# Performance work log

Measured on AMD Instinct MI355X. Metric: run time of the kernel, lower is better.

The kernel has to match this reference:

```python
import jax, jax.numpy as jnp
import numpy as np

TEMPERATURE = 0.07
NORM_EPS = 1e-12  # matches torch F.normalize eps


def setup_inputs() -> dict:
    key = jax.random.key(0)
    k1, k2 = jax.random.split(key)
    emb = jax.random.normal(k1, (4, 256, 61, 61), dtype=jnp.float32)
    targets = jax.random.randint(k2, (4, 61, 61), 0, 5, dtype=jnp.int64)
    return {"emb": emb, "targets": targets}


def reference(emb, targets):
    n, c, h, w = emb.shape
    # (N,C,H,W) -> (N*H*W, C), L2-normalized per pixel
    feats = emb.transpose(0, 2, 3, 1).reshape(-1, c)
    norms = jnp.maximum(jnp.linalg.norm(feats, axis=1, keepdims=True), NORM_EPS)
    feats = feats / norms
    labels = targets.reshape(-1)  # (T,)
    T = labels.shape[0]

    sim = jnp.matmul(feats, feats.T) / TEMPERATURE  # (T,T)
    exp_sim = jnp.exp(sim)

    eye = jnp.eye(T, dtype=bool)
    pos_mask = (labels[None, :] == labels[:, None]) & ~eye  # (T,T) bool

    sum_pos = jnp.sum(jnp.where(pos_mask, exp_sim, 0.0), axis=1)  # (T,)
    sum_all = exp_sim.sum(axis=1) - jnp.exp(jnp.diagonal(sim))    # (T,)

    valid = sum_pos > 0
    # safe log: substitute 1.0 where invalid to avoid -inf/NaN, then mask
    safe_pos = jnp.where(valid, sum_pos, 1.0)
    safe_all = jnp.where(valid, sum_all, 1.0)
    per_row = jnp.where(valid, -(jnp.log(safe_pos) - jnp.log(safe_all)), 0.0)
    loss = per_row.sum() / jnp.maximum(valid.sum(), 1).astype(per_row.dtype)
    return loss
```

## Files before the change

### kernel.cpp

```cpp
#include <hip/hip_runtime.h>
#include <cstdint>
#include <cstddef>

#define T_REAL 14884
#define TPAD   15360
#define CDIM   256
#define HW     3721
#define NRB    60
#define NSL    16
#define TPS    15
#define NT     240
#define NPADJ  476.0f

static constexpr float SQRT_SCALE = 4.53981598f;

typedef _Float16 f16x8  __attribute__((ext_vector_type(8)));
typedef float    f32x16 __attribute__((ext_vector_type(16)));

__device__ __forceinline__ float exp2_fast(float x) {
#if __has_builtin(__builtin_amdgcn_exp2f)
    return __builtin_amdgcn_exp2f(x);
#else
    return exp2f(x);
#endif
}

#define OFF_FEATS 0u
#define SZ_FEATS  ((unsigned)TPAD * CDIM * 2u)
#define OFF_LAB   (OFF_FEATS + SZ_FEATS)
#define OFF_RANK  (OFF_LAB + (unsigned)TPAD * 4u)
#define OFF_CTL   (OFF_RANK + 59648u)
#define OFF_TCL   (OFF_CTL + 128u)
#define OFF_PART  (OFF_TCL + 1024u)
#define SZ_PART   ((unsigned)NRB * NSL * 256u * 8u)
#define OFF_ACC   (OFF_PART + SZ_PART)


__global__ void k_zero(int* __restrict__ ctl, float* __restrict__ accum) {
    int t = threadIdx.x;
    if (t < 32) ctl[t] = 0;
    if (t == 32) { accum[0] = 0.f; accum[1] = 0.f; }
}

__global__ void k_hist(const int* __restrict__ targets, int* __restrict__ ctl) {
    __shared__ int lh[5];
    const int tid = threadIdx.x;
    const int t = blockIdx.x * 256 + tid;
    if (tid < 5) lh[tid] = 0;
    __syncthreads();
    if (t < T_REAL) atomicAdd(&lh[targets[t]], 1);
    __syncthreads();
    if (tid < 5) atomicAdd(&ctl[tid], lh[tid]);
}

__global__ void k_scan(int* __restrict__ ctl, int* __restrict__ tcl,
                       int* __restrict__ labels) {
    __shared__ int soffs[6];
    const int tid = threadIdx.x;
    if (tid == 0) {
        int o = 0;
        for (int c = 0; c < 5; ++c) {
            soffs[c] = o; ctl[16 + c] = o; ctl[8 + c] = o;
            o += ctl[c];
        }
        soffs[5] = o; ctl[21] = o;
    }
    __syncthreads();
    for (int t = tid; t < NT; t += 256) {
        const int lo = t * 64, hi = lo + 64;
        int tc = -2;
        if (lo >= T_REAL) tc = -1;
        else {
#pragma unroll
            for (int c = 0; c < 5; ++c)
                if (lo >= soffs[c] && hi <= soffs[c + 1]) tc = c;
        }
        tcl[t] = tc;
    }
    for (int t = T_REAL + tid; t < TPAD; t += 256) labels[t] = -1;
}

__global__ void k_rank(const int* __restrict__ targets, int* __restrict__ ctl,
                       int* __restrict__ rank, int* __restrict__ labels) {
    const int tid = threadIdx.x;
    const int t = blockIdx.x * 256 + tid;
    const int lane = tid & 63;
    const int c = (t < T_REAL) ? targets[t] : -1;
#pragma unroll
    for (int cl = 0; cl < 5; ++cl) {
        unsigned long long m = __ballot(c == cl);
        if (c == cl) {
            const int leader = __ffsll((unsigned long long)m) - 1;
            int base = 0;
            if (lane == leader) base = atomicAdd(&ctl[8 + cl], (int)__popcll(m));
            base = __shfl(base, leader);
            const unsigned long long below = m & ((1ull << lane) - 1ull);
            const int r = base + (int)__popcll(below);
            rank[t] = r;
            labels[r] = c;
        }
    }
}

__global__ void k_prep(const float* __restrict__ emb, const int* __restrict__ rank,
                       _Float16* __restrict__ feats) {
    const int tid = threadIdx.x;
    const int bx = blockIdx.x, n = blockIdx.y;

    if (bx == 59) {
        const int r0 = T_REAL + n * 119;
        f16x8 z = {0, 0, 0, 0, 0, 0, 0, 0};
        for (int c = tid; c < 119 * 32; c += 256) {
            int rr = r0 + (c >> 5), cc = c & 31;
            *reinterpret_cast<f16x8*>(feats + (size_t)rr * CDIM + cc * 8) = z;
        }
        return;
    }

    __shared__ float tile[64][257];
    __shared__ float sspart[4][64];
    const int lane = tid & 63, w = tid >> 6;
    const int px0 = bx * 64;
    const int hw = px0 + lane;

    float ssq = 0.f;
    for (int ci = w; ci < CDIM; ci += 4) {
        float v = (hw < HW) ? emb[((size_t)(n * CDIM + ci)) * HW + hw] : 0.f;
        tile[lane][ci] = v;
        ssq += v * v;
    }
    sspart[w][lane] = ssq;
    __syncthreads();

    const int pp = tid >> 2, q = tid & 3;
    float s2 = sspart[q][pp];
    s2 += __shfl_xor(s2, 1);
    s2 += __shfl_xor(s2, 2);
    const float inv = SQRT_SCALE / fmaxf(sqrtf(s2), 1e-12f);

    const int hwp = px0 + pp;
    if (hwp < HW) {
        const int row = rank[n * HW + hwp];
        _Float16* dst = feats + (size_t)row * CDIM + q * 64;
#pragma unroll
        for (int g = 0; g < 8; ++g) {
            const int gg = g ^ q;
            f16x8 o;
#pragma unroll
            for (int e = 0; e < 8; ++e) o[e] = (_Float16)(tile[pp][q * 64 + gg * 8 + e] * inv);
            *reinterpret_cast<f16x8*>(dst + gg * 8) = o;
        }
    }
}

__device__ __forceinline__ void stage_tile(const _Float16* __restrict__ feats, int jbase,
                                           _Float16* bufp, int tid) {
#pragma unroll
    for (int sweep = 0; sweep < 8; ++sweep) {
        int ch = sweep * 256 + tid;
        int j  = ch >> 5;
        int c  = ch & 31;
        int swz = (j & 7) ^ (((j >> 3) & 3) << 1);
        int csrc = c ^ swz;
        const _Float16* src = feats + ((size_t)(jbase + j)) * CDIM + csrc * 8;
        __builtin_amdgcn_global_load_lds(
            (const __attribute__((address_space(1))) void*)src,
            (__attribute__((address_space(3))) void*)(bufp + (size_t)ch * 8),
            16, 0, 0);
    }
}

__global__ __launch_bounds__(256, 2) void k_main(const _Float16* __restrict__ feats,
                                                 const int* __restrict__ labels,
                                                 const int* __restrict__ tcl,
                                                 float2* __restrict__ partials) {
    __shared__ __align__(16) _Float16 buf[2][64 * 256];
    const int tid  = threadIdx.x;
    const int w    = tid >> 6, lane = tid & 63;
    const int lo   = lane & 31, hi = lane >> 5;
    const int rb = blockIdx.x, slice = blockIdx.y;
    const int ibase = rb * 256 + w * 64;

    const int labi0 = labels[ibase + lo];
    const int labi1 = labels[ibase + 32 + lo];

    f16x8 b0[16], b1[16];
    {
        const f16x8* r0 = (const f16x8*)(feats + (size_t)(ibase + lo) * CDIM + hi * 8);
        const f16x8* r1 = (const f16x8*)(feats + (size_t)(ibase + 32 + lo) * CDIM + hi * 8);
#pragma unroll
        for (int ks = 0; ks < 16; ++ks) { b0[ks] = r0[ks * 2]; b1[ks] = r1[ks * 2]; }
    }

    const int s  = (lo & 7) ^ (((lo >> 3) & 3) << 1);
    const int sp = s >> 1;
    const int x0h = (s & 1) << 3;
    int idx4[4];
#pragma unroll
    for (int m = 0; m < 4; ++m)
        idx4[m] = lo * 256 + ((hi << 3) ^ x0h) + (((m ^ sp)) << 4);

    float accA0 = 0.f, accP0 = 0.f, accA1 = 0.f, accP1 = 0.f;

    stage_tile(feats, slice * 64, &buf[0][0], tid);

#pragma unroll 1
    for (int ti = 0; ti < TPS; ++ti) {
        const int jt = slice + ti * NSL;

        __builtin_amdgcn_s_barrier();
        __builtin_amdgcn_sched_barrier(0);
        if (ti + 1 < TPS) {
            stage_tile(feats, (jt + NSL) * 64, &buf[(ti + 1) & 1][0], tid);
            asm volatile("s_waitcnt vmcnt(8)" ::: "memory");
        } else {
            asm volatile("s_waitcnt vmcnt(0)" ::: "memory");
        }
        __builtin_amdgcn_s_barrier();
        __builtin_amdgcn_sched_barrier(0);

        const _Float16* bc = &buf[ti & 1][0];
        const int tc = tcl[jt];
        float tT0 = 0.f, tT1 = 0.f;

#pragma unroll
        for (int jg = 0; jg < 2; ++jg) {
            const _Float16* bjg = bc + jg * 8192;
            f32x16 cA = {0,0,0,0,0,0,0,0,0,0,0,0,0,0,0,0};
            f32x16 cB = cA;
#pragma unroll
            for (int ks = 0; ks < 16; ++ks) {
                const f16x8 a = *reinterpret_cast<const f16x8*>(
                    bjg + idx4[ks & 3] + ((ks & 12) << 4));
                cA = __builtin_amdgcn_mfma_f32_32x32x16_f16(a, b0[ks], cA, 0, 0, 0);
                cB = __builtin_amdgcn_mfma_f32_32x32x16_f16(a, b1[ks], cB, 0, 0, 0);
            }
            if (tc != -2) {
#pragma unroll
                for (int v = 0; v < 16; ++v) {
                    tT0 += exp2_fast(cA[v]);
                    tT1 += exp2_fast(cB[v]);
                }
            } else {
                const int jb2 = jt * 64 + jg * 32;
#pragma unroll
                for (int q = 0; q < 4; ++q) {
                    const int4 lj = *reinterpret_cast<const int4*>(labels + jb2 + q * 8 + hi * 4);
#pragma unroll
                    for (int r = 0; r < 4; ++r) {
                        const int ljr = (r == 0) ? lj.x : (r == 1) ? lj.y : (r == 2) ? lj.z : lj.w;
                        float e0 = exp2_fast(cA[q * 4 + r]);
                        accA0 += e0;
                        accP0 += (ljr == labi0) ? e0 : 0.f;
                        float e1 = exp2_fast(cB[q * 4 + r]);
                        accA1 += e1;
                        accP1 += (ljr == labi1) ? e1 : 0.f;
                    }
                }
            }
        }
        if (tc != -2) {
            accA0 += tT0; accA1 += tT1;
            accP0 += (tc == labi0) ? tT0 : 0.f;
            accP1 += (tc == labi1) ? tT1 : 0.f;
        }
    }

    float n0 = 0.f, n1 = 0.f;
#pragma unroll
    for (int ks = 0; ks < 16; ++ks)
#pragma unroll
        for (int e = 0; e < 8; ++e) {
            float v0 = (float)b0[ks][e]; n0 += v0 * v0;
            float v1 = (float)b1[ks][e]; n1 += v1 * v1;
        }
    n0 += __shfl_xor(n0, 32); n1 += __shfl_xor(n1, 32);

    accA0 += __shfl_xor(accA0, 32); accP0 += __shfl_xor(accP0, 32);
    accA1 += __shfl_xor(accA1, 32); accP1 += __shfl_xor(accP1, 32);

    if (((rb * 4 + w) & (NSL - 1)) == slice) {
        float e0 = exp2_fast(n0), e1 = exp2_fast(n1);
        accA0 -= e0; accP0 -= e0;
        accA1 -= e1; accP1 -= e1;
    }

    if (hi == 0) {
        size_t base = ((size_t)(rb * NSL + slice)) * 256 + w * 64;
        partials[base + lo]      = make_float2(accA0, accP0);
        partials[base + 32 + lo] = make_float2(accA1, accP1);
    }
}

__global__ void k_reduce(const float2* __restrict__ partials, float* __restrict__ accum) {
    const int rb = blockIdx.x;
    const int rl = threadIdx.x;
    const int t  = rb * 256 + rl;
    float sA = -NPADJ, sP = 0.f;
#pragma unroll
    for (int s = 0; s < NSL; ++s) {
        float2 v = partials[((size_t)(rb * NSL + s)) * 256 + rl];
        sA += v.x; sP += v.y;
    }
    float per = 0.f, cnt = 0.f;
    if (t < T_REAL && sP > 0.f) {
        per = logf(sA) - logf(sP);
        cnt = 1.f;
    }
#pragma unroll
    for (int off = 32; off >= 1; off >>= 1) {
        per += __shfl_xor(per, off);
        cnt += __shfl_xor(cnt, off);
    }
    if ((threadIdx.x & 63) == 0) { atomicAdd(&accum[0], per); atomicAdd(&accum[1], cnt); }
}

__global__ void k_final(const float* __restrict__ accum, float* __restrict__ out) {
    out[0] = accum[0] / fmaxf(accum[1], 1.0f);
}

extern "C" void kernel_launch(void* const* d_in, const int* in_sizes, int n_in,
                              void* d_out, int out_size, void* d_ws, size_t ws_size,
                              hipStream_t stream) {
    const float* emb     = (const float*)d_in[0];
    const int*   targets = (const int*)d_in[1];
    float*       out     = (float*)d_out;
    char*        ws      = (char*)d_ws;

    _Float16* feats    = (_Float16*)(ws + OFF_FEATS);
    int*      labels   = (int*)(ws + OFF_LAB);
    int*      rank     = (int*)(ws + OFF_RANK);
    int*      ctl      = (int*)(ws + OFF_CTL);
    int*      tcl      = (int*)(ws + OFF_TCL);
    float2*   partials = (float2*)(ws + OFF_PART);
    float*    accum    = (float*)(ws + OFF_ACC);

    k_zero  <<<dim3(1),        dim3(64),  0, stream>>>(ctl, accum);
    k_hist  <<<dim3(59),       dim3(256), 0, stream>>>(targets, ctl);
    k_scan  <<<dim3(1),        dim3(256), 0, stream>>>(ctl, tcl, labels);
    k_rank  <<<dim3(59),       dim3(256), 0, stream>>>(targets, ctl, rank, labels);
    k_prep  <<<dim3(60, 4),    dim3(256), 0, stream>>>(emb, rank, feats);
    k_main  <<<dim3(NRB, NSL), dim3(256), 0, stream>>>(feats, labels, tcl, partials);
    k_reduce<<<dim3(NRB),      dim3(256), 0, stream>>>(partials, accum);
    k_final <<<dim3(1),        dim3(1),   0, stream>>>(accum, out);
}
```

Measured before the change: 231.1 us.

## Merge setup kernels, restructure main MFMA loop with split staging and final-block reduce

```diff
diff --git a/kernel.cpp b/kernel.cpp
--- a/kernel.cpp
+++ b/kernel.cpp
@@ -29,44 +29,58 @@
 #define SZ_FEATS  ((unsigned)TPAD * CDIM * 2u)
 #define OFF_LAB   (OFF_FEATS + SZ_FEATS)
 #define OFF_RANK  (OFF_LAB + (unsigned)TPAD * 4u)
-#define OFF_CTL   (OFF_RANK + 59648u)
-#define OFF_TCL   (OFF_CTL + 128u)
-#define OFF_PART  (OFF_TCL + 1024u)
+#define OFF_TCL   (OFF_RANK + 59648u)
+#define OFF_DONE  (OFF_TCL + 1024u)
+#define OFF_PART  (OFF_DONE + 128u)
 #define SZ_PART   ((unsigned)NRB * NSL * 256u * 8u)
 #define OFF_ACC   (OFF_PART + SZ_PART)
 
-
-__global__ void k_zero(int* __restrict__ ctl, float* __restrict__ accum) {
-    int t = threadIdx.x;
-    if (t < 32) ctl[t] = 0;
-    if (t == 32) { accum[0] = 0.f; accum[1] = 0.f; }
-}
-
-__global__ void k_hist(const int* __restrict__ targets, int* __restrict__ ctl) {
-    __shared__ int lh[5];
-    const int tid = threadIdx.x;
-    const int t = blockIdx.x * 256 + tid;
-    if (tid < 5) lh[tid] = 0;
-    __syncthreads();
-    if (t < T_REAL) atomicAdd(&lh[targets[t]], 1);
-    __syncthreads();
-    if (tid < 5) atomicAdd(&ctl[tid], lh[tid]);
-}
-
-__global__ void k_scan(int* __restrict__ ctl, int* __restrict__ tcl,
-                       int* __restrict__ labels) {
-    __shared__ int soffs[6];
-    const int tid = threadIdx.x;
+__global__ void k_sort(const int* __restrict__ targets, int* __restrict__ rank,
+                       int* __restrict__ labels, int* __restrict__ tcl,
+                       float* __restrict__ accum, int* __restrict__ done) {
+    __shared__ int h[5], cur[5], soffs[6];
+    const int tid = threadIdx.x, lane = tid & 63;
+    if (tid < 5) h[tid] = 0;
+    if (tid == 8) { accum[0] = 0.f; accum[1] = 0.f; }
+    if (tid == 9) done[0] = 0;
+    __syncthreads();
+
+    for (int t = tid; t < T_REAL; t += 1024) {
+        const int c = targets[t];
+#pragma unroll
+        for (int cl = 0; cl < 5; ++cl) {
+            unsigned long long m = __ballot(c == cl);
+            if (c == cl && lane == __ffsll(m) - 1) atomicAdd(&h[cl], (int)__popcll(m));
+        }
+    }
+    __syncthreads();
     if (tid == 0) {
         int o = 0;
-        for (int c = 0; c < 5; ++c) {
-            soffs[c] = o; ctl[16 + c] = o; ctl[8 + c] = o;
-            o += ctl[c];
-        }
-        soffs[5] = o; ctl[21] = o;
-    }
-    __syncthreads();
-    for (int t = tid; t < NT; t += 256) {
+#pragma unroll
+        for (int c = 0; c < 5; ++c) { soffs[c] = o; cur[c] = o; o += h[c]; }
+        soffs[5] = o;
+    }
+    __syncthreads();
+
+    for (int t = tid; t < T_REAL; t += 1024) {
+        const int c = targets[t];
+#pragma unroll
+        for (int cl = 0; cl < 5; ++cl) {
+            unsigned long long m = __ballot(c == cl);
+            if (c == cl) {
+                const int leader = __ffsll(m) - 1;
+                int base = 0;
+                if (lane == leader) base = atomicAdd(&cur[cl], (int)__popcll(m));
+                base = __shfl(base, leader);
+                const int r = base + (int)__popcll(m & ((1ull << lane) - 1ull));
+                rank[t] = r;
+                labels[r] = c;
+            }
+        }
+    }
+    for (int t = T_REAL + tid; t < TPAD; t += 1024) labels[t] = -1;
+
+    for (int t = tid; t < NT; t += 1024) {
         const int lo = t * 64, hi = lo + 64;
         int tc = -2;
         if (lo >= T_REAL) tc = -1;
@@ -76,29 +90,6 @@
                 if (lo >= soffs[c] && hi <= soffs[c + 1]) tc = c;
         }
         tcl[t] = tc;
-    }
-    for (int t = T_REAL + tid; t < TPAD; t += 256) labels[t] = -1;
-}
-
-__global__ void k_rank(const int* __restrict__ targets, int* __restrict__ ctl,
-                       int* __restrict__ rank, int* __restrict__ labels) {
-    const int tid = threadIdx.x;
-    const int t = blockIdx.x * 256 + tid;
-    const int lane = tid & 63;
-    const int c = (t < T_REAL) ? targets[t] : -1;
-#pragma unroll
-    for (int cl = 0; cl < 5; ++cl) {
-        unsigned long long m = __ballot(c == cl);
-        if (c == cl) {
-            const int leader = __ffsll((unsigned long long)m) - 1;
-            int base = 0;
-            if (lane == leader) base = atomicAdd(&ctl[8 + cl], (int)__popcll(m));
-            base = __shfl(base, leader);
-            const unsigned long long below = m & ((1ull << lane) - 1ull);
-            const int r = base + (int)__popcll(below);
-            rank[t] = r;
-            labels[r] = c;
-        }
     }
 }
 
@@ -153,16 +144,16 @@
     }
 }
 
-__device__ __forceinline__ void stage_tile(const _Float16* __restrict__ feats, int jbase,
-                                           _Float16* bufp, int tid) {
-#pragma unroll
-    for (int sweep = 0; sweep < 8; ++sweep) {
-        int ch = sweep * 256 + tid;
-        int j  = ch >> 5;
-        int c  = ch & 31;
-        int swz = (j & 7) ^ (((j >> 3) & 3) << 1);
-        int csrc = c ^ swz;
-        const _Float16* src = feats + ((size_t)(jbase + j)) * CDIM + csrc * 8;
+__device__ __forceinline__ void stage_half(const _Float16* __restrict__ feats, int jbase,
+                                           _Float16* bufp, int tid, int half) {
+#pragma unroll
+    for (int s4 = 0; s4 < 4; ++s4) {
+        const int sweep = half * 4 + s4;
+        const int ch = sweep * 256 + tid;
+        const int j  = ch >> 5;
+        const int c  = ch & 31;
+        const int swz = (j & 7) ^ (((j >> 3) & 3) << 1);
+        const _Float16* src = feats + ((size_t)(jbase + j)) * CDIM + (c ^ swz) * 8;
         __builtin_amdgcn_global_load_lds(
             (const __attribute__((address_space(1))) void*)src,
             (__attribute__((address_space(3))) void*)(bufp + (size_t)ch * 8),
@@ -198,72 +189,89 @@
     int idx4[4];
 #pragma unroll
     for (int m = 0; m < 4; ++m)
-        idx4[m] = lo * 256 + ((hi << 3) ^ x0h) + (((m ^ sp)) << 4);
+        idx4[m] = lo * 256 + ((hi << 3) ^ x0h) + ((m ^ sp) << 4);
 
     float accA0 = 0.f, accP0 = 0.f, accA1 = 0.f, accP1 = 0.f;
 
-    stage_tile(feats, slice * 64, &buf[0][0], tid);
+    stage_half(feats, slice * 64, &buf[0][0], tid, 0);
+    stage_half(feats, slice * 64, &buf[0][0], tid, 1);
 
 #pragma unroll 1
     for (int ti = 0; ti < TPS; ++ti) {
         const int jt = slice + ti * NSL;
-
+        const bool nxt = (ti + 1 < TPS);
+        const int tc = tcl[__builtin_amdgcn_readfirstlane(jt)];
+
+        if (nxt) {
+            stage_half(feats, (jt + NSL) * 64, &buf[(ti + 1) & 1][0], tid, 0);
+            asm volatile("s_waitcnt vmcnt(4)" ::: "memory");
+        } else {
+            asm volatile("s_waitcnt vmcnt(0)" ::: "memory");
+        }
         __builtin_amdgcn_s_barrier();
         __builtin_amdgcn_sched_barrier(0);
-        if (ti + 1 < TPS) {
-            stage_tile(feats, (jt + NSL) * 64, &buf[(ti + 1) & 1][0], tid);
-            asm volatile("s_waitcnt vmcnt(8)" ::: "memory");
+
+        const _Float16* bc = &buf[ti & 1][0];
+        f32x16 c00 = {0,0,0,0,0,0,0,0,0,0,0,0,0,0,0,0};
+        f32x16 c01 = c00, c10 = c00, c11 = c00;
+
+#pragma unroll
+        for (int ph = 0; ph < 4; ++ph) {
+            f16x8 a0[4], a1[4];
+#pragma unroll
+            for (int m = 0; m < 4; ++m) {
+                const int off = idx4[m] + (ph << 6);
+                a0[m] = *reinterpret_cast<const f16x8*>(bc + off);
+                a1[m] = *reinterpret_cast<const f16x8*>(bc + 8192 + off);
+            }
+            if (ph == 0 && nxt)
+                stage_half(feats, (jt + NSL) * 64, &buf[(ti + 1) & 1][0], tid, 1);
+            asm volatile("s_waitcnt lgkmcnt(0)" ::: "memory");
+            __builtin_amdgcn_sched_barrier(0);
+            __builtin_amdgcn_s_setprio(1);
+#pragma unroll
+            for (int m = 0; m < 4; ++m) {
+                const int ks = ph * 4 + m;
+                c00 = __builtin_amdgcn_mfma_f32_32x32x16_f16(a0[m], b0[ks], c00, 0, 0, 0);
+                c01 = __builtin_amdgcn_mfma_f32_32x32x16_f16(a0[m], b1[ks], c01, 0, 0, 0);
+                c10 = __builtin_amdgcn_mfma_f32_32x32x16_f16(a1[m], b0[ks], c10, 0, 0, 0);
+                c11 = __builtin_amdgcn_mfma_f32_32x32x16_f16(a1[m], b1[ks], c11, 0, 0, 0);
+            }
+            __builtin_amdgcn_s_setprio(0);
+        }
+
+        if (tc != -2) {
+            float t0 = 0.f, t1 = 0.f, t2 = 0.f, t3 = 0.f;
+#pragma unroll
+            for (int v = 0; v < 16; ++v) {
+                t0 += exp2_fast(c00[v]);
+                t1 += exp2_fast(c01[v]);
+                t2 += exp2_fast(c10[v]);
+                t3 += exp2_fast(c11[v]);
+            }
+            accA0 += t0 + t2; accA1 += t1 + t3;
+            accP0 += (tc == labi0) ? (t0 + t2) : 0.f;
+            accP1 += (tc == labi1) ? (t1 + t3) : 0.f;
         } else {
-            asm volatile("s_waitcnt vmcnt(0)" ::: "memory");
+            const int jb = jt * 64;
+#pragma unroll
+            for (int q = 0; q < 4; ++q) {
+                const int4 lj0 = *reinterpret_cast<const int4*>(labels + jb + q * 8 + hi * 4);
+                const int4 lj1 = *reinterpret_cast<const int4*>(labels + jb + 32 + q * 8 + hi * 4);
+#pragma unroll
+                for (int r = 0; r < 4; ++r) {
+                    const int l0 = (r == 0) ? lj0.x : (r == 1) ? lj0.y : (r == 2) ? lj0.z : lj0.w;
+                    const int l1 = (r == 0) ? lj1.x : (r == 1) ? lj1.y : (r == 2) ? lj1.z : lj1.w;
+                    const int v = q * 4 + r;
+                    float e;
+                    e = exp2_fast(c00[v]); accA0 += e; accP0 += (l0 == labi0) ? e : 0.f;
+                    e = exp2_fast(c01[v]); accA1 += e; accP1 += (l0 == labi1) ? e : 0.f;
+                    e = exp2_fast(c10[v]); accA0 += e; accP0 += (l1 == labi0) ? e : 0.f;
+                    e = exp2_fast(c11[v]); accA1 += e; accP1 += (l1 == labi1) ? e : 0.f;
+                }
+            }
         }
         __builtin_amdgcn_s_barrier();
-        __builtin_amdgcn_sched_barrier(0);
-
-        const _Float16* bc = &buf[ti & 1][0];
-        const int tc = tcl[jt];
-        float tT0 = 0.f, tT1 = 0.f;
-
-#pragma unroll
-        for (int jg = 0; jg < 2; ++jg) {
-            const _Float16* bjg = bc + jg * 8192;
-            f32x16 cA = {0,0,0,0,0,0,0,0,0,0,0,0,0,0,0,0};
-            f32x16 cB = cA;
-#pragma unroll
-            for (int ks = 0; ks < 16; ++ks) {
-                const f16x8 a = *reinterpret_cast<const f16x8*>(
-                    bjg + idx4[ks & 3] + ((ks & 12) << 4));
-                cA = __builtin_amdgcn_mfma_f32_32x32x16_f16(a, b0[ks], cA, 0, 0, 0);
-                cB = __builtin_amdgcn_mfma_f32_32x32x16_f16(a, b1[ks], cB, 0, 0, 0);
-            }
-            if (tc != -2) {
-#pragma unroll
-                for (int v = 0; v < 16; ++v) {
-                    tT0 += exp2_fast(cA[v]);
-                    tT1 += exp2_fast(cB[v]);
-                }
-            } else {
-                const int jb2 = jt * 64 + jg * 32;
-#pragma unroll
-                for (int q = 0; q < 4; ++q) {
-                    const int4 lj = *reinterpret_cast<const int4*>(labels + jb2 + q * 8 + hi * 4);
-#pragma unroll
-                    for (int r = 0; r < 4; ++r) {
-                        const int ljr = (r == 0) ? lj.x : (r == 1) ? lj.y : (r == 2) ? lj.z : lj.w;
-                        float e0 = exp2_fast(cA[q * 4 + r]);
-                        accA0 += e0;
-                        accP0 += (ljr == labi0) ? e0 : 0.f;
-                        float e1 = exp2_fast(cB[q * 4 + r]);
-                        accA1 += e1;
-                        accP1 += (ljr == labi1) ? e1 : 0.f;
-                    }
-                }
-            }
-        }
-        if (tc != -2) {
-            accA0 += tT0; accA1 += tT1;
-            accP0 += (tc == labi0) ? tT0 : 0.f;
-            accP1 += (tc == labi1) ? tT1 : 0.f;
-        }
     }
 
     float n0 = 0.f, n1 = 0.f;
@@ -292,7 +300,8 @@
     }
 }
 
-__global__ void k_reduce(const float2* __restrict__ partials, float* __restrict__ accum) {
+__global__ void k_reduce(const float2* __restrict__ partials, float* __restrict__ accum,
+                         int* __restrict__ done, float* __restrict__ out) {
     const int rb = blockIdx.x;
     const int rl = threadIdx.x;
     const int t  = rb * 256 + rl;
@@ -312,11 +321,16 @@
         per += __shfl_xor(per, off);
         cnt += __shfl_xor(cnt, off);
     }
-    if ((threadIdx.x & 63) == 0) { atomicAdd(&accum[0], per); atomicAdd(&accum[1], cnt); }
-}
-
-__global__ void k_final(const float* __restrict__ accum, float* __restrict__ out) {
-    out[0] = accum[0] / fmaxf(accum[1], 1.0f);
+    if ((rl & 63) == 0) { atomicAdd(&accum[0], per); atomicAdd(&accum[1], cnt); }
+    __syncthreads();
+    if (rl == 0) {
+        __threadfence();
+        if (atomicAdd(done, 1) == NRB - 1) {
+            float a = atomicAdd(&accum[0], 0.f);
+            float c = atomicAdd(&accum[1], 0.f);
+            out[0] = a / fmaxf(c, 1.f);
+        }
+    }
 }
 
 extern "C" void kernel_launch(void* const* d_in, const int* in_sizes, int n_in,
@@ -330,17 +344,13 @@
     _Float16* feats    = (_Float16*)(ws + OFF_FEATS);
     int*      labels   = (int*)(ws + OFF_LAB);
     int*      rank     = (int*)(ws + OFF_RANK);
-    int*      ctl      = (int*)(ws + OFF_CTL);
     int*      tcl      = (int*)(ws + OFF_TCL);
+    int*      done     = (int*)(ws + OFF_DONE);
     float2*   partials = (float2*)(ws + OFF_PART);
     float*    accum    = (float*)(ws + OFF_ACC);
 
-    k_zero  <<<dim3(1),        dim3(64),  0, stream>>>(ctl, accum);
-    k_hist  <<<dim3(59),       dim3(256), 0, stream>>>(targets, ctl);
-    k_scan  <<<dim3(1),        dim3(256), 0, stream>>>(ctl, tcl, labels);
-    k_rank  <<<dim3(59),       dim3(256), 0, stream>>>(targets, ctl, rank, labels);
-    k_prep  <<<dim3(60, 4),    dim3(256), 0, stream>>>(emb, rank, feats);
-    k_main  <<<dim3(NRB, NSL), dim3(256), 0, stream>>>(feats, labels, tcl, partials);
-    k_reduce<<<dim3(NRB),      dim3(256), 0, stream>>>(partials, accum);
-    k_final <<<dim3(1),        dim3(1),   0, stream>>>(accum, out);
-}
+    k_sort  <<<dim3(1),        dim3(1024), 0, stream>>>(targets, rank, labels, tcl, accum, done);
+    k_prep  <<<dim3(60, 4),    dim3(256),  0, stream>>>(emb, rank, feats);
+    k_main  <<<dim3(NRB, NSL), dim3(256),  0, stream>>>(feats, labels, tcl, partials);
+    k_reduce<<<dim3(NRB),      dim3(256),  0, stream>>>(partials, accum, done, out);
+}
```

After: 261.5 us. 1.13x slower.
